# Kernel optimization log

Hardware: AMD Instinct MI355X
Metric: run time of the kernel (lower is better)

## Reference

```python
import math
import jax, jax.numpy as jnp
import numpy as np

D, H, L, DFF, V = 512, 8, 6, 2048, 32000
B, S = 2, 2048
PAD = 1


def _layernorm(x, g, b, eps=1e-5):
    m = x.mean(-1, keepdims=True)
    v = ((x - m) ** 2).mean(-1, keepdims=True)
    return (x - m) / jnp.sqrt(v + eps) * g + b


def _mha(qx, kx, w, b, mask, h=H):
    # w: [4, D, D] (q,k,v,out), b: [4, D]; mask broadcastable to [B,1,Sq,Sk]
    bs, sq, d = qx.shape
    dk = d // h
    def proj(x, i):
        return (x @ w[i] + b[i]).reshape(bs, -1, h, dk).transpose(0, 2, 1, 3)
    q, k, v = proj(qx, 0), proj(kx, 1), proj(kx, 2)
    scores = jnp.einsum('bhqd,bhkd->bhqk', q, k) / math.sqrt(dk)
    scores = jnp.where(mask, scores, -jnp.inf)
    attn = jax.nn.softmax(scores, axis=-1)
    out = jnp.einsum('bhqk,bhkd->bhqd', attn, v).transpose(0, 2, 1, 3).reshape(bs, sq, d)
    return out @ w[3] + b[3]


def _ff(x, w1, b1, w2, b2):
    return jax.nn.relu(x @ w1 + b1) @ w2 + b2


def _sinusoidal_pe(max_len, d):
    pos = np.arange(max_len)[:, None].astype(np.float64)
    div = np.exp(np.arange(0, d, 2) * (-math.log(10000.0) / d))
    pe = np.zeros((max_len, d), np.float32)
    pe[:, 0::2] = np.sin(pos * div)
    pe[:, 1::2] = np.cos(pos * div)
    return jnp.asarray(pe[None])  # [1, max_len, d]


def setup_inputs() -> dict:
    key = jax.random.key(0)
    ks = iter(jax.random.split(key, 32))
    def w(shape):
        return jax.random.normal(next(ks), shape, jnp.float32) * 0.02
    inp = {
        'src': jax.random.randint(next(ks), (B, S), 2, V),
        'tgt': jax.random.randint(next(ks), (B, S), 2, V),
        'src_emb': w((V, D)),
        'tgt_emb': w((V, D)),
        'pe': _sinusoidal_pe(S, D),
        'enc_attn_w': w((L, 4, D, D)), 'enc_attn_b': jnp.zeros((L, 4, D)),
        'enc_ff_w1': w((L, D, DFF)), 'enc_ff_b1': jnp.zeros((L, DFF)),
        'enc_ff_w2': w((L, DFF, D)), 'enc_ff_b2': jnp.zeros((L, D)),
        'enc_ln_g': jnp.ones((L, 2, D)), 'enc_ln_b': jnp.zeros((L, 2, D)),
        'dec_self_w': w((L, 4, D, D)), 'dec_self_b': jnp.zeros((L, 4, D)),
        'dec_src_w': w((L, 4, D, D)), 'dec_src_b': jnp.zeros((L, 4, D)),
        'dec_ff_w1': w((L, D, DFF)), 'dec_ff_b1': jnp.zeros((L, DFF)),
        'dec_ff_w2': w((L, DFF, D)), 'dec_ff_b2': jnp.zeros((L, D)),
        'dec_ln_g': jnp.ones((L, 3, D)), 'dec_ln_b': jnp.zeros((L, 3, D)),
        'ln_g': jnp.ones((D,)), 'ln_b': jnp.zeros((D,)),
        'fc_w': w((D, V)), 'fc_b': jnp.zeros((V,)),
    }
    return inp


def reference(src, tgt, src_emb, tgt_emb, pe,
              enc_attn_w, enc_attn_b, enc_ff_w1, enc_ff_b1, enc_ff_w2, enc_ff_b2,
              enc_ln_g, enc_ln_b,
              dec_self_w, dec_self_b, dec_src_w, dec_src_b,
              dec_ff_w1, dec_ff_b1, dec_ff_w2, dec_ff_b2, dec_ln_g, dec_ln_b,
              ln_g, ln_b, fc_w, fc_b):
    s_len, t_len = src.shape[1], tgt.shape[1]
    src_mask = (src != PAD)[:, None, None, :]                      # [B,1,1,Ss]
    tril = jnp.tril(jnp.ones((t_len, t_len), bool))
    tgt_mask = (tgt != PAD)[:, None, None, :] & tril[None, None]   # [B,1,St,St]

    x = src_emb[src] + pe[:, :s_len]
    for l in range(L):
        x2 = _layernorm(x, enc_ln_g[l, 0], enc_ln_b[l, 0])
        x = x + _mha(x2, x2, enc_attn_w[l], enc_attn_b[l], src_mask)
        x2 = _layernorm(x, enc_ln_g[l, 1], enc_ln_b[l, 1])
        x = x + _ff(x2, enc_ff_w1[l], enc_ff_b1[l], enc_ff_w2[l], enc_ff_b2[l])
    memory = x

    y = tgt_emb[tgt] + pe[:, :t_len]
    for l in range(L):
        y2 = _layernorm(y, dec_ln_g[l, 0], dec_ln_b[l, 0])
        y = y + _mha(y2, y2, dec_self_w[l], dec_self_b[l], tgt_mask)
        y2 = _layernorm(y, dec_ln_g[l, 1], dec_ln_b[l, 1])
        y = y + _mha(y2, memory, dec_src_w[l], dec_src_b[l], src_mask)
        y2 = _layernorm(y, dec_ln_g[l, 2], dec_ln_b[l, 2])
        y = y + _ff(y2, dec_ff_w1[l], dec_ff_b1[l], dec_ff_w2[l], dec_ff_b2[l])

    return _layernorm(y, ln_g, ln_b) @ fc_w + fc_b  # [B, St, V]
```

## Files before the change

### kernel.cpp

```cpp
#include <hip/hip_runtime.h>
#include <math.h>

#define D_MODEL 512
#define NHEAD   8
#define NLAYER  6
#define DFF_    2048
#define VOCAB   32000
#define BATCH   2
#define SEQ     2048
#define NTOK    (BATCH*SEQ)
#define PAD_ID  1

typedef __attribute__((ext_vector_type(8))) short s16x8;
typedef __attribute__((ext_vector_type(4))) float f32x4;
typedef unsigned short u16;
typedef unsigned int   u32;
typedef unsigned long long u64;

__device__ __forceinline__ u16 f2bf(float x) {
  u32 u = __builtin_bit_cast(u32, x);
  u += 0x7FFFu + ((u >> 16) & 1u);
  return (u16)(u >> 16);
}

__device__ __forceinline__ float exp2i(float x) {
  float r; asm("v_exp_f32 %0, %1" : "=v"(r) : "v"(x)); return r;
}

__device__ __forceinline__ void gload16(const void* g, void* l) {
  __builtin_amdgcn_global_load_lds(
      (const __attribute__((address_space(1))) u32*)g,
      (__attribute__((address_space(3))) u32*)l, 16, 0, 0);
}

#define CEXP 0.1803368802f

__global__ __launch_bounds__(256) void embed2_kernel(
    const int* __restrict__ src, const int* __restrict__ tgt,
    const float* __restrict__ se, const float* __restrict__ te,
    const float* __restrict__ pe, float* __restrict__ xe, float* __restrict__ yd)
{
  const int z = blockIdx.y;
  const int* tok = z ? tgt : src;
  const float* emb = z ? te : se;
  float* out = z ? yd : xe;
  const int total = NTOK * D_MODEL;
  for (int i = blockIdx.x * 256 + threadIdx.x; i < total; i += gridDim.x * 256) {
    int t = i >> 9;
    int d = i & 511;
    int s = t & (SEQ - 1);
    out[i] = emb[(size_t)tok[t] * D_MODEL + d] + pe[(size_t)s * D_MODEL + d];
  }
}

__global__ __launch_bounds__(64) void padmask2_kernel(
    const int* __restrict__ src, const int* __restrict__ tgt,
    u64* __restrict__ pmS, u64* __restrict__ pmT)
{
  const int z = blockIdx.z;
  const int* tok = z ? tgt : src;
  u64* pm = z ? pmT : pmS;
  int b = blockIdx.y, t = blockIdx.x;
  int lane = threadIdx.x;
  u64 m = __ballot(tok[(size_t)b * SEQ + t * 64 + lane] != PAD_ID);
  if (lane == 0) pm[b * (SEQ / 64) + t] = m;
}

__global__ __launch_bounds__(256) void ln_kernel(
    const float* __restrict__ x, const float* __restrict__ g,
    const float* __restrict__ bb, u16* __restrict__ y)
{
  __shared__ float red[8];
  const size_t row = blockIdx.x;
  const float* xr = x + row * D_MODEL;
  u16* yr = y + row * D_MODEL;
  const int t = threadIdx.x;
  float a0 = xr[t], a1 = xr[t + 256];
  float s = a0 + a1;
  #pragma unroll
  for (int o = 32; o > 0; o >>= 1) s += __shfl_down(s, o, 64);
  int wv = t >> 6, ln = t & 63;
  if (ln == 0) red[wv] = s;
  __syncthreads();
  if (t == 0) red[4] = red[0] + red[1] + red[2] + red[3];
  __syncthreads();
  float mean = red[4] * (1.0f / D_MODEL);
  float d0 = a0 - mean, d1 = a1 - mean;
  float vs = d0 * d0 + d1 * d1;
  #pragma unroll
  for (int o = 32; o > 0; o >>= 1) vs += __shfl_down(vs, o, 64);
  if (ln == 0) red[wv] = vs;
  __syncthreads();
  if (t == 0) red[5] = red[0] + red[1] + red[2] + red[3];
  __syncthreads();
  float inv = rsqrtf(red[5] * (1.0f / D_MODEL) + 1e-5f);
  yr[t]       = f2bf(d0 * inv * g[t]       + bb[t]);
  yr[t + 256] = f2bf(d1 * inv * g[t + 256] + bb[t + 256]);
}

__global__ __launch_bounds__(256) void tconv2_kernel(
    const float* __restrict__ s0, const float* __restrict__ s1,
    u16* __restrict__ d0, u16* __restrict__ d1, int zsplit, int K, int N)
{
  __shared__ float tile[64][65];
  const int z = blockIdx.z;
  const float* src = (z < zsplit) ? s0 + (size_t)z * K * N : s1 + (size_t)(z - zsplit) * K * N;
  u16* dst = (z < zsplit) ? d0 + (size_t)z * K * N : d1 + (size_t)(z - zsplit) * K * N;
  const int n0 = blockIdx.x * 64, k0 = blockIdx.y * 64;
  const int t = threadIdx.x;
  const int cr = t >> 4, cc = (t & 15) * 4;
  #pragma unroll
  for (int it = 0; it < 4; ++it) {
    int kr = cr + it * 16;
    float4 v = *(const float4*)&src[(size_t)(k0 + kr) * N + n0 + cc];
    tile[kr][cc] = v.x; tile[kr][cc + 1] = v.y; tile[kr][cc + 2] = v.z; tile[kr][cc + 3] = v.w;
  }
  __syncthreads();
  #pragma unroll
  for (int it = 0; it < 4; ++it) {
    int nr = cr + it * 16;
    u32 lo = (u32)f2bf(tile[cc + 0][nr]) | ((u32)f2bf(tile[cc + 1][nr]) << 16);
    u32 hi = (u32)f2bf(tile[cc + 2][nr]) | ((u32)f2bf(tile[cc + 3][nr]) << 16);
    uint2 pk; pk.x = lo; pk.y = hi;
    *(uint2*)&dst[(size_t)(n0 + nr) * K + k0 + cc] = pk;
  }
}

template<int MODE, int BM, int BN, int MAP>
__global__ __launch_bounds__(256, 2) void mm_kernel(
    const u16* __restrict__ A, const u16* __restrict__ Wt,
    const float* __restrict__ bias, const float* __restrict__ res,
    void* __restrict__ Cout, u16* __restrict__ vtOut,
    int M, int N, int K,
    long long wStride, long long bStride, long long cStride)
{
  constexpr int MI = BM / 32;
  constexpr int NI = BN / 32;
  constexpr bool DB = (BM == 64 && BN == 64);
  __shared__ u16 sh[(DB ? 2 : 1) * (BM + BN) * 64];
  const int z = blockIdx.z;
  size_t wOff, bOff;
  if (MAP == 1) {
    wOff = (size_t)(z >> 1) * 4 * 262144 + (size_t)(1 + (z & 1)) * 262144;
    bOff = (size_t)(z >> 1) * 4 * 512 + (size_t)(1 + (z & 1)) * 512;
  } else {
    wOff = (size_t)z * wStride;
    bOff = (size_t)z * bStride;
  }
  Wt += wOff;
  bias += bOff;
  const int bm = blockIdx.y * BM, bn = blockIdx.x * BN;
  const int tid = threadIdx.x, lane = tid & 63, w = tid >> 6;
  const int wm = w >> 1, wn = w & 1;
  const int l15 = lane & 15, l4 = lane >> 4;
  const int wrow0 = wm * (BM / 2), wcol0 = wn * (BN / 2);
  const u16* aBase = A  + (size_t)bm * K;
  const u16* bBase = Wt + (size_t)bn * K;
  f32x4 acc[MI][NI] = {};

  auto mfma_step = [&](const u16* Asb, const u16* Bsb) {
    #pragma unroll
    for (int ks = 0; ks < 2; ++ks) {
      s16x8 af[MI], bf[NI];
      #pragma unroll
      for (int mi = 0; mi < MI; ++mi) {
        int rr = wrow0 + mi * 16 + l15;
        af[mi] = *(const s16x8*)&Asb[(rr << 6) + (((ks * 4 + l4) ^ (rr & 7)) << 3)];
      }
      #pragma unroll
      for (int ni = 0; ni < NI; ++ni) {
        int rr = wcol0 + ni * 16 + l15;
        bf[ni] = *(const s16x8*)&Bsb[(rr << 6) + (((ks * 4 + l4) ^ (rr & 7)) << 3)];
      }
      #pragma unroll
      for (int mi = 0; mi < MI; ++mi)
        #pragma unroll
        for (int ni = 0; ni < NI; ++ni)
          acc[mi][ni] = __builtin_amdgcn_mfma_f32_16x16x32_bf16(af[mi], bf[ni], acc[mi][ni], 0, 0, 0);
    }
  };

  if constexpr (DB) {
    u16* As0 = sh;
    u16* As1 = sh + 64 * 64;
    u16* Bs0 = sh + 2 * 64 * 64;
    u16* Bs1 = sh + 3 * 64 * 64;
    auto stage = [&](int k0, u16* Ad, u16* Bd) {
      #pragma unroll
      for (int i = 0; i < 2; ++i) {
        int lin = i * 256 + tid;
        int r = lin >> 3, sp = lin & 7;
        gload16(aBase + (size_t)r * K + k0 + ((sp ^ (r & 7)) * 8), &Ad[(i * 256 + w * 64) * 8]);
      }
      #pragma unroll
      for (int i = 0; i < 2; ++i) {
        int lin = i * 256 + tid;
        int r = lin >> 3, sp = lin & 7;
        gload16(bBase + (size_t)r * K + k0 + ((sp ^ (r & 7)) * 8), &Bd[(i * 256 + w * 64) * 8]);
      }
    };
    stage(0, As0, Bs0);
    __syncthreads();
    const int nt = K >> 6;
    for (int t = 0; t < nt; ++t) {
      const bool even = !(t & 1);
      u16* Ac = even ? As0 : As1;
      u16* Bc = even ? Bs0 : Bs1;
      if (t + 1 < nt) stage((t + 1) << 6, even ? As1 : As0, even ? Bs1 : Bs0);
      mfma_step(Ac, Bc);
      __syncthreads();
    }
  } else {
    u16* As = sh;
    u16* Bs = sh + BM * 64;
    for (int k0 = 0; k0 < K; k0 += 64) {
      #pragma unroll
      for (int i = 0; i < BM / 32; ++i) {
        int lin = i * 256 + tid;
        int r = lin >> 3, sp = lin & 7;
        gload16(aBase + (size_t)r * K + k0 + ((sp ^ (r & 7)) * 8), &As[(i * 256 + w * 64) * 8]);
      }
      #pragma unroll
      for (int i = 0; i < BN / 32; ++i) {
        int lin = i * 256 + tid;
        int r = lin >> 3, sp = lin & 7;
        gload16(bBase + (size_t)r * K + k0 + ((sp ^ (r & 7)) * 8), &Bs[(i * 256 + w * 64) * 8]);
      }
      __syncthreads();
      mfma_step(As, Bs);
      __syncthreads();
    }
  }

  const bool vpath = (MODE == 4 && z == 2) || (MODE == 5 && (z & 1) == 1);
  if (vpath) {
    u16* TT = sh;
    #pragma unroll
    for (int mi = 0; mi < MI; ++mi)
      #pragma unroll
      for (int ni = 0; ni < NI; ++ni)
        #pragma unroll
        for (int r = 0; r < 4; ++r) {
          int rowl = wrow0 + mi * 16 + l4 * 4 + r;
          int coll = wcol0 + ni * 16 + l15;
          TT[coll * 72 + rowl] = f2bf(acc[mi][ni][r] + bias[bn + coll]);
        }
    __syncthreads();
    const int b = bm >> 11, s0loc = bm & 2047, h = bn >> 6;
    const int layer = (MODE == 5) ? (z >> 1) : 0;
    u16* vbase = vtOut + (size_t)layer * ((size_t)NTOK * D_MODEL)
               + ((size_t)(b * NHEAD + h) * 64) * SEQ;
    int d = tid >> 2, sc = (tid & 3) * 16;
    s16x8 v0 = *(const s16x8*)&TT[d * 72 + sc];
    s16x8 v1 = *(const s16x8*)&TT[d * 72 + sc + 8];
    *(s16x8*)(vbase + (size_t)d * SEQ + s0loc + sc) = v0;
    *(s16x8*)(vbase + (size_t)d * SEQ + s0loc + sc + 8) = v1;
    return;
  }

  const int zi = (MAP == 1) ? (z >> 1) : z;
  #pragma unroll
  for (int ni = 0; ni < NI; ++ni) {
    int col = bn + wcol0 + ni * 16 + l15;
    float bb = bias[col];
    #pragma unroll
    for (int mi = 0; mi < MI; ++mi) {
      #pragma unroll
      for (int r = 0; r < 4; ++r) {
        int row = bm + wrow0 + mi * 16 + l4 * 4 + r;
        size_t off = (size_t)zi * cStride + (size_t)row * N + col;
        float v = acc[mi][ni][r] + bb;
        if (MODE == 1 || MODE == 6) v += res[(size_t)row * N + col];
        if (MODE == 3) v = fmaxf(v, 0.0f);
        if (MODE <= 1 || MODE == 6) ((float*)Cout)[off] = v;
        else                        ((u16*)Cout)[off] = f2bf(v);
        if (MODE == 6) vtOut[(size_t)row * N + col] = f2bf(v);
      }
    }
  }
}

template<int CAUSAL>
__global__ __launch_bounds__(256, 2) void fattn_kernel(
    const u16* __restrict__ Qg, const u16* __restrict__ Kg,
    const u16* __restrict__ Vt, const u64* __restrict__ padm,
    u16* __restrict__ Og)
{
  __shared__ u16 Ks[2][128 * 64];
  __shared__ u16 Vs[2][64 * 128];
  __shared__ u16 Ps[4][16 * 128];
  const int qtile = CAUSAL ? (int)(gridDim.x - 1 - blockIdx.x) : (int)blockIdx.x;
  const int qt = qtile * 64;
  const int h = blockIdx.y, b = blockIdx.z;
  const int tid = threadIdx.x, lane = tid & 63, w = tid >> 6;
  const int l15 = lane & 15, l4 = lane >> 4;
  const int hoff = h * 64;
  const u16* Kbase = Kg + (size_t)(b * SEQ) * D_MODEL + hoff;
  const u16* Vbase = Vt + (size_t)(b * NHEAD + h) * 64 * SEQ;
  const u64* pmb = padm + b * (SEQ / 64);

  s16x8 aq[2];
  {
    const u16* qp = Qg + (size_t)(b * SEQ + qt + w * 16 + l15) * D_MODEL + hoff + l4 * 8;
    aq[0] = *(const s16x8*)qp;
    aq[1] = *(const s16x8*)(qp + 32);
  }

  f32x4 oacc[4] = {};
  float mrow[4] = {-1e30f, -1e30f, -1e30f, -1e30f};
  float lrow[4] = {0.f, 0.f, 0.f, 0.f};
  const int nt = CAUSAL ? (qt >> 7) + 1 : SEQ / 128;

  #define STAGE(KV0, BUF)                                                              \
    {                                                                                  \
      _Pragma("unroll")                                                                \
      for (int it = 0; it < 4; ++it) {                                                 \
        int lin = it * 256 + tid;                                                      \
        int rr = lin >> 3, sp = lin & 7;                                               \
        gload16(Kbase + (size_t)((KV0) + rr) * D_MODEL + ((sp ^ (rr & 7)) * 8),        \
                &Ks[BUF][(it * 256 + w * 64) * 8]);                                    \
      }                                                                                \
      _Pragma("unroll")                                                                \
      for (int it = 0; it < 4; ++it) {                                                 \
        int lin = it * 256 + tid;                                                      \
        int rr = lin >> 4, ko = lin & 15;                                              \
        gload16(Vbase + (size_t)rr * SEQ + (KV0) + ((ko ^ (rr & 15)) * 8),             \
                &Vs[BUF][(it * 256 + w * 64) * 8]);                                    \
      }                                                                                \
    }

  STAGE(0, 0);
  __syncthreads();

  for (int kt = 0; kt < nt; ++kt) {
    const int kv0 = kt * 128;
    const int cur = kt & 1;
    if (kt + 1 < nt) STAGE(kv0 + 128, cur ^ 1);

    f32x4 sac[8] = {};
    #pragma unroll
    for (int ks = 0; ks < 2; ++ks)
      #pragma unroll
      for (int jn = 0; jn < 8; ++jn) {
        int rr = jn * 16 + l15;
        s16x8 bk = *(const s16x8*)&Ks[cur][(rr << 6) + (((ks * 4 + l4) ^ (rr & 7)) << 3)];
        sac[jn] = __builtin_amdgcn_mfma_f32_16x16x32_bf16(aq[ks], bk, sac[jn], 0, 0, 0);
      }

    const u64 m0 = pmb[(kv0 >> 6)];
    const u64 m1 = pmb[(kv0 >> 6) + 1];
    const bool lastC = CAUSAL && (kt == nt - 1);
    if (((m0 & m1) != ~0ull) || lastC) {
      #pragma unroll
      for (int jn = 0; jn < 8; ++jn) {
        int kvg = kv0 + jn * 16 + l15;
        u64 mm = (jn < 4) ? m0 : m1;
        bool okp = (mm >> ((jn & 3) * 16 + l15)) & 1;
        #pragma unroll
        for (int r = 0; r < 4; ++r) {
          int qg = qt + w * 16 + l4 * 4 + r;
          bool ok = okp && (!CAUSAL || kvg <= qg);
          if (!ok) sac[jn][r] = -1e30f;
        }
      }
    }

    float mx[4];
    #pragma unroll
    for (int r = 0; r < 4; ++r) {
      float m = fmaxf(fmaxf(fmaxf(sac[0][r], sac[1][r]), fmaxf(sac[2][r], sac[3][r])),
                      fmaxf(fmaxf(sac[4][r], sac[5][r]), fmaxf(sac[6][r], sac[7][r])));
      #pragma unroll
      for (int o = 1; o < 16; o <<= 1) m = fmaxf(m, __shfl_xor(m, o, 16));
      mx[r] = m;
    }
    float growth = fmaxf(fmaxf(mx[0] - mrow[0], mx[1] - mrow[1]),
                         fmaxf(mx[2] - mrow[2], mx[3] - mrow[3]));
    if (__any(growth > 64.0f)) {
      #pragma unroll
      for (int r = 0; r < 4; ++r) {
        float mn = fmaxf(mrow[r], mx[r]);
        float sc = exp2i((mrow[r] - mn) * CEXP);
        mrow[r] = mn;
        lrow[r] *= sc;
        #pragma unroll
        for (int jn = 0; jn < 4; ++jn) oacc[jn][r] *= sc;
      }
    }

    #pragma unroll
    for (int r = 0; r < 4; ++r) {
      const int prow = l4 * 4 + r;
      float rs = 0.f;
      #pragma unroll
      for (int jn = 0; jn < 8; ++jn) {
        float pv = exp2i((sac[jn][r] - mrow[r]) * CEXP);
        rs += pv;
        int g = ((jn * 2 + (l15 >> 3)) ^ prow) & 15;
        Ps[w][prow * 128 + g * 8 + (l15 & 7)] = f2bf(pv);
      }
      #pragma unroll
      for (int o = 1; o < 16; o <<= 1) rs += __shfl_xor(rs, o, 16);
      lrow[r] += rs;
    }

    #pragma unroll
    for (int kslot = 0; kslot < 4; ++kslot) {
      s16x8 pa = *(const s16x8*)&Ps[w][l15 * 128 + ((((kslot * 4 + l4) ^ l15) & 15) << 3)];
      #pragma unroll
      for (int jn = 0; jn < 4; ++jn) {
        int rr = jn * 16 + l15;
        s16x8 bv = *(const s16x8*)&Vs[cur][(rr << 7) + (((kslot * 4 + l4) ^ (rr & 15)) << 3)];
        oacc[jn] = __builtin_amdgcn_mfma_f32_16x16x32_bf16(pa, bv, oacc[jn], 0, 0, 0);
      }
    }
    __syncthreads();
  }
  #undef STAGE

  float inv[4];
  #pragma unroll
  for (int r = 0; r < 4; ++r) inv[r] = 1.0f / lrow[r];
  #pragma unroll
  for (int jn = 0; jn < 4; ++jn)
    #pragma unroll
    for (int r = 0; r < 4; ++r)
      Og[(size_t)(b * SEQ + qt + w * 16 + l4 * 4 + r) * D_MODEL + hoff + jn * 16 + l15] =
          f2bf(oacc[jn][r] * inv[r]);
}

extern "C" void kernel_launch(void* const* d_in, const int* in_sizes, int n_in,
                              void* d_out, int out_size, void* d_ws, size_t ws_size,
                              hipStream_t stream)
{
  const int*   src        = (const int*)  d_in[0];
  const int*   tgt        = (const int*)  d_in[1];
  const float* src_emb    = (const float*)d_in[2];
  const float* tgt_emb    = (const float*)d_in[3];
  const float* pe         = (const float*)d_in[4];
  const float* enc_attn_w = (const float*)d_in[5];
  const float* enc_attn_b = (const float*)d_in[6];
  const float* enc_ff_w1  = (const float*)d_in[7];
  const float* enc_ff_b1  = (const float*)d_in[8];
  const float* enc_ff_w2  = (const float*)d_in[9];
  const float* enc_ff_b2  = (const float*)d_in[10];
  const float* enc_ln_g   = (const float*)d_in[11];
  const float* enc_ln_bb  = (const float*)d_in[12];
  const float* dec_self_w = (const float*)d_in[13];
  const float* dec_self_b = (const float*)d_in[14];
  const float* dec_src_w  = (const float*)d_in[15];
  const float* dec_src_b  = (const float*)d_in[16];
  const float* dec_ff_w1  = (const float*)d_in[17];
  const float* dec_ff_b1  = (const float*)d_in[18];
  const float* dec_ff_w2  = (const float*)d_in[19];
  const float* dec_ff_b2  = (const float*)d_in[20];
  const float* dec_ln_g   = (const float*)d_in[21];
  const float* dec_ln_bb  = (const float*)d_in[22];
  const float* fin_ln_g   = (const float*)d_in[23];
  const float* fin_ln_b   = (const float*)d_in[24];
  const float* fc_w       = (const float*)d_in[25];
  const float* fc_b       = (const float*)d_in[26];
  float* out = (float*)d_out;

  const size_t DD = (size_t)D_MODEL * D_MODEL;
  const size_t FD = (size_t)D_MODEL * DFF_;
  const size_t TD = (size_t)NTOK * D_MODEL;

  char* ob = (char*)d_out;
  size_t off = 0;
  auto alloco = [&](size_t bytes) { void* p = ob + off; off += (bytes + 255) & ~(size_t)255; return p; };
  u16* wt_enc_attn = (u16*)alloco(24 * DD * 2);
  u16* wt_dec_self = (u16*)alloco(24 * DD * 2);
  u16* wt_dec_src  = (u16*)alloco(24 * DD * 2);
  u16* wt_enc_ff1  = (u16*)alloco(6 * FD * 2);
  u16* wt_enc_ff2  = (u16*)alloco(6 * FD * 2);
  u16* wt_dec_ff1  = (u16*)alloco(6 * FD * 2);
  u16* wt_dec_ff2  = (u16*)alloco(6 * FD * 2);
  u16* qb   = (u16*)alloco(2 * TD * 2);
  u16* kb   = qb + TD;
  u16* vtb  = (u16*)alloco(TD * 2);
  u16* aob  = (u16*)alloco(TD * 2);
  u16* hbb  = (u16*)alloco((size_t)NTOK * DFF_ * 2);
  u16* memb = (u16*)alloco(TD * 2);
  u16* ckb  = (u16*)alloco(6 * TD * 2);
  u16* cvtb = (u16*)alloco(6 * TD * 2);

  char* wsb = (char*)d_ws;
  u16*   fcwt = (u16*)wsb;
  size_t wo = ((size_t)VOCAB * D_MODEL * 2 + 255) & ~(size_t)255;
  float* xe  = (float*)(wsb + wo); wo += TD * 4;
  float* yd  = (float*)(wsb + wo); wo += TD * 4;
  u16*   x2b = (u16*)(wsb + wo);   wo += TD * 2;
  u64*   pmS = (u64*)(wsb + wo);   wo += 1024;
  u64*   pmT = (u64*)(wsb + wo);

  dim3 blk(256);
  dim3 gN512(8, 64, 1), gQKV(8, 64, 3), gCKV(8, 64, 12);
  dim3 gFF1(16, 32, 1), gFC(250, 32, 1);
  dim3 gAttn(SEQ / 64, NHEAD, BATCH);
  const long long llDD = (long long)DD, llTD = (long long)TD;

  padmask2_kernel<<<dim3(SEQ / 64, BATCH, 2), dim3(64), 0, stream>>>(src, tgt, pmS, pmT);
  tconv2_kernel<<<dim3(8, 8, 48), blk, 0, stream>>>(enc_attn_w, dec_self_w, wt_enc_attn, wt_dec_self, 24, 512, 512);
  tconv2_kernel<<<dim3(8, 8, 24), blk, 0, stream>>>(dec_src_w, dec_src_w, wt_dec_src, wt_dec_src, 24, 512, 512);
  tconv2_kernel<<<dim3(32, 8, 12), blk, 0, stream>>>(enc_ff_w1, dec_ff_w1, wt_enc_ff1, wt_dec_ff1, 6, 512, 2048);
  tconv2_kernel<<<dim3(8, 32, 12), blk, 0, stream>>>(enc_ff_w2, dec_ff_w2, wt_enc_ff2, wt_dec_ff2, 6, 2048, 512);
  tconv2_kernel<<<dim3(500, 8, 1), blk, 0, stream>>>(fc_w, fc_w, fcwt, fcwt, 1, 512, VOCAB);
  embed2_kernel<<<dim3(2048, 2), blk, 0, stream>>>(src, tgt, src_emb, tgt_emb, pe, xe, yd);

  for (int l = 0; l < NLAYER; ++l) {
    ln_kernel<<<dim3(NTOK), blk, 0, stream>>>(xe, enc_ln_g + (size_t)(l * 2 + 0) * D_MODEL,
                                              enc_ln_bb + (size_t)(l * 2 + 0) * D_MODEL, x2b);
    mm_kernel<4, 64, 64, 0><<<gQKV, blk, 0, stream>>>(x2b, wt_enc_attn + (size_t)l * 4 * DD,
        enc_attn_b + (size_t)l * 4 * D_MODEL, nullptr, qb, vtb, NTOK, 512, 512, llDD, D_MODEL, llTD);
    fattn_kernel<0><<<gAttn, blk, 0, stream>>>(qb, kb, vtb, pmS, aob);
    mm_kernel<1, 64, 64, 0><<<gN512, blk, 0, stream>>>(aob, wt_enc_attn + (size_t)(l * 4 + 3) * DD,
        enc_attn_b + (size_t)(l * 4 + 3) * D_MODEL, xe, xe, nullptr, NTOK, 512, 512, 0, 0, 0);
    ln_kernel<<<dim3(NTOK), blk, 0, stream>>>(xe, enc_ln_g + (size_t)(l * 2 + 1) * D_MODEL,
                                              enc_ln_bb + (size_t)(l * 2 + 1) * D_MODEL, x2b);
    mm_kernel<3, 128, 128, 0><<<gFF1, blk, 0, stream>>>(x2b, wt_enc_ff1 + (size_t)l * FD,
        enc_ff_b1 + (size_t)l * DFF_, nullptr, hbb, nullptr, NTOK, DFF_, 512, 0, 0, 0);
    if (l == NLAYER - 1)
      mm_kernel<6, 64, 64, 0><<<gN512, blk, 0, stream>>>(hbb, wt_enc_ff2 + (size_t)l * FD,
          enc_ff_b2 + (size_t)l * D_MODEL, xe, xe, memb, NTOK, 512, DFF_, 0, 0, 0);
    else
      mm_kernel<1, 64, 64, 0><<<gN512, blk, 0, stream>>>(hbb, wt_enc_ff2 + (size_t)l * FD,
          enc_ff_b2 + (size_t)l * D_MODEL, xe, xe, nullptr, NTOK, 512, DFF_, 0, 0, 0);
  }

  mm_kernel<5, 64, 64, 1><<<gCKV, blk, 0, stream>>>(memb, wt_dec_src, dec_src_b, nullptr,
      ckb, cvtb, NTOK, 512, 512, 0, 0, llTD);

  for (int l = 0; l < NLAYER; ++l) {
    const u16* Ws = wt_dec_self + (size_t)l * 4 * DD;
    const u16* Wc = wt_dec_src + (size_t)l * 4 * DD;
    const float* bs  = dec_self_b + (size_t)l * 4 * D_MODEL;
    const float* bcb = dec_src_b + (size_t)l * 4 * D_MODEL;
    ln_kernel<<<dim3(NTOK), blk, 0, stream>>>(yd, dec_ln_g + (size_t)(l * 3 + 0) * D_MODEL,
                                              dec_ln_bb + (size_t)(l * 3 + 0) * D_MODEL, x2b);
    mm_kernel<4, 64, 64, 0><<<gQKV, blk, 0, stream>>>(x2b, Ws, bs, nullptr, qb, vtb,
                                                      NTOK, 512, 512, llDD, D_MODEL, llTD);
    fattn_kernel<1><<<gAttn, blk, 0, stream>>>(qb, kb, vtb, pmT, aob);
    mm_kernel<1, 64, 64, 0><<<gN512, blk, 0, stream>>>(aob, Ws + 3 * DD, bs + 3 * D_MODEL, yd, yd,
                                                       nullptr, NTOK, 512, 512, 0, 0, 0);
    ln_kernel<<<dim3(NTOK), blk, 0, stream>>>(yd, dec_ln_g + (size_t)(l * 3 + 1) * D_MODEL,
                                              dec_ln_bb + (size_t)(l * 3 + 1) * D_MODEL, x2b);
    mm_kernel<2, 64, 64, 0><<<gN512, blk, 0, stream>>>(x2b, Wc, bcb, nullptr, qb, nullptr,
                                                       NTOK, 512, 512, 0, 0, 0);
    fattn_kernel<0><<<gAttn, blk, 0, stream>>>(qb, ckb + (size_t)l * TD, cvtb + (size_t)l * TD,
                                               pmS, aob);
    mm_kernel<1, 64, 64, 0><<<gN512, blk, 0, stream>>>(aob, Wc + 3 * DD, bcb + 3 * D_MODEL, yd, yd,
                                                       nullptr, NTOK, 512, 512, 0, 0, 0);
    ln_kernel<<<dim3(NTOK), blk, 0, stream>>>(yd, dec_ln_g + (size_t)(l * 3 + 2) * D_MODEL,
                                              dec_ln_bb + (size_t)(l * 3 + 2) * D_MODEL, x2b);
    mm_kernel<3, 128, 128, 0><<<gFF1, blk, 0, stream>>>(x2b, wt_dec_ff1 + (size_t)l * FD,
        dec_ff_b1 + (size_t)l * DFF_, nullptr, hbb, nullptr, NTOK, DFF_, 512, 0, 0, 0);
    mm_kernel<1, 64, 64, 0><<<gN512, blk, 0, stream>>>(hbb, wt_dec_ff2 + (size_t)l * FD,
        dec_ff_b2 + (size_t)l * D_MODEL, yd, yd, nullptr, NTOK, 512, DFF_, 0, 0, 0);
  }

  ln_kernel<<<dim3(NTOK), blk, 0, stream>>>(yd, fin_ln_g, fin_ln_b, x2b);
  mm_kernel<0, 128, 128, 0><<<gFC, blk, 0, stream>>>(x2b, fcwt, fc_b, nullptr, out, nullptr,
                                                     NTOK, VOCAB, 512, 0, 0, 0);

  (void)in_sizes; (void)n_in; (void)out_size; (void)ws_size;
}
```

Measured before the change: 2.504 ms.

## Fuse cross-attn Q projection into attention, merge weight transposes, widen FC tile

The decoder cross-attention Q projection is now computed inside the flash-attention kernel from the normalized activations and the per-head weight slice, which removes a separate GEMM launch and the Q round trip through global memory. The three attention-weight transpose launches are merged into one kernel, which assumes the three weight buffers are contiguous in the destination. The final vocab projection uses 128x256 tiles with half the grid. Risks include extra per-block work and shared-memory syncs in the attention prologue, and higher register pressure from the wider FC tile.

```diff
diff --git a/kernel.cpp b/kernel.cpp
--- a/kernel.cpp
+++ b/kernel.cpp
@@ -123,6 +123,36 @@
     u32 hi = (u32)f2bf(tile[cc + 2][nr]) | ((u32)f2bf(tile[cc + 3][nr]) << 16);
     uint2 pk; pk.x = lo; pk.y = hi;
     *(uint2*)&dst[(size_t)(n0 + nr) * K + k0 + cc] = pk;
+  }
+}
+
+__global__ __launch_bounds__(256) void tconv3_kernel(
+    const float* __restrict__ s0, const float* __restrict__ s1,
+    const float* __restrict__ s2, u16* __restrict__ dst0)
+{
+  __shared__ float tile[64][65];
+  const int z = blockIdx.z;
+  const float* src = (z < 24) ? s0 + (size_t)z * 262144
+                   : (z < 48) ? s1 + (size_t)(z - 24) * 262144
+                              : s2 + (size_t)(z - 48) * 262144;
+  u16* dst = dst0 + (size_t)z * 262144;
+  const int n0 = blockIdx.x * 64, k0 = blockIdx.y * 64;
+  const int t = threadIdx.x;
+  const int cr = t >> 4, cc = (t & 15) * 4;
+  #pragma unroll
+  for (int it = 0; it < 4; ++it) {
+    int kr = cr + it * 16;
+    float4 v = *(const float4*)&src[(size_t)(k0 + kr) * 512 + n0 + cc];
+    tile[kr][cc] = v.x; tile[kr][cc + 1] = v.y; tile[kr][cc + 2] = v.z; tile[kr][cc + 3] = v.w;
+  }
+  __syncthreads();
+  #pragma unroll
+  for (int it = 0; it < 4; ++it) {
+    int nr = cr + it * 16;
+    u32 lo = (u32)f2bf(tile[cc + 0][nr]) | ((u32)f2bf(tile[cc + 1][nr]) << 16);
+    u32 hi = (u32)f2bf(tile[cc + 2][nr]) | ((u32)f2bf(tile[cc + 3][nr]) << 16);
+    uint2 pk; pk.x = lo; pk.y = hi;
+    *(uint2*)&dst[(size_t)(n0 + nr) * 512 + k0 + cc] = pk;
   }
 }
 
@@ -280,10 +310,11 @@
   }
 }
 
-template<int CAUSAL>
+template<int CAUSAL, int QPROJ>
 __global__ __launch_bounds__(256, 2) void fattn_kernel(
     const u16* __restrict__ Qg, const u16* __restrict__ Kg,
-    const u16* __restrict__ Vt, const u64* __restrict__ padm,
+    const u16* __restrict__ Vt, const u16* __restrict__ Wq,
+    const float* __restrict__ qbias, const u64* __restrict__ padm,
     u16* __restrict__ Og)
 {
   __shared__ u16 Ks[2][128 * 64];
@@ -300,7 +331,57 @@
   const u64* pmb = padm + b * (SEQ / 64);
 
   s16x8 aq[2];
-  {
+  if constexpr (QPROJ) {
+    const u16* xBase = Qg + (size_t)(b * SEQ + qt) * D_MODEL;
+    const u16* wBase = Wq + (size_t)hoff * D_MODEL;
+    u16* Xs = Ks[0];
+    u16* Wsh = Ks[0] + 64 * 64;
+    f32x4 qa[4] = {};
+    for (int k0 = 0; k0 < 512; k0 += 64) {
+      #pragma unroll
+      for (int i = 0; i < 2; ++i) {
+        int lin = i * 256 + tid;
+        int r = lin >> 3, sp = lin & 7;
+        gload16(xBase + (size_t)r * D_MODEL + k0 + ((sp ^ (r & 7)) * 8), &Xs[(i * 256 + w * 64) * 8]);
+      }
+      #pragma unroll
+      for (int i = 0; i < 2; ++i) {
+        int lin = i * 256 + tid;
+        int r = lin >> 3, sp = lin & 7;
+        gload16(wBase + (size_t)r * D_MODEL + k0 + ((sp ^ (r & 7)) * 8), &Wsh[(i * 256 + w * 64) * 8]);
+      }
+      __syncthreads();
+      #pragma unroll
+      for (int ks = 0; ks < 2; ++ks) {
+        int rr = w * 16 + l15;
+        s16x8 xa = *(const s16x8*)&Xs[(rr << 6) + (((ks * 4 + l4) ^ (rr & 7)) << 3)];
+        #pragma unroll
+        for (int ni = 0; ni < 4; ++ni) {
+          int rw = ni * 16 + l15;
+          s16x8 wb = *(const s16x8*)&Wsh[(rw << 6) + (((ks * 4 + l4) ^ (rw & 7)) << 3)];
+          qa[ni] = __builtin_amdgcn_mfma_f32_16x16x32_bf16(xa, wb, qa[ni], 0, 0, 0);
+        }
+      }
+      __syncthreads();
+    }
+    u16* Qsh = (u16*)Ps;
+    #pragma unroll
+    for (int ni = 0; ni < 4; ++ni) {
+      int col = ni * 16 + l15;
+      float bb = qbias[hoff + col];
+      #pragma unroll
+      for (int r = 0; r < 4; ++r) {
+        int row = w * 16 + l4 * 4 + r;
+        Qsh[(row << 6) + ((((col >> 3)) ^ (row & 7)) << 3) + (col & 7)] = f2bf(qa[ni][r] + bb);
+      }
+    }
+    __syncthreads();
+    {
+      int rr = w * 16 + l15;
+      aq[0] = *(const s16x8*)&Qsh[(rr << 6) + (((0 + l4) ^ (rr & 7)) << 3)];
+      aq[1] = *(const s16x8*)&Qsh[(rr << 6) + (((4 + l4) ^ (rr & 7)) << 3)];
+    }
+  } else {
     const u16* qp = Qg + (size_t)(b * SEQ + qt + w * 16 + l15) * D_MODEL + hoff + l4 * 8;
     aq[0] = *(const s16x8*)qp;
     aq[1] = *(const s16x8*)(qp + 32);
@@ -329,6 +410,7 @@
       }                                                                                \
     }
 
+  if constexpr (QPROJ) __syncthreads();
   STAGE(0, 0);
   __syncthreads();
 
@@ -496,13 +578,12 @@
 
   dim3 blk(256);
   dim3 gN512(8, 64, 1), gQKV(8, 64, 3), gCKV(8, 64, 12);
-  dim3 gFF1(16, 32, 1), gFC(250, 32, 1);
+  dim3 gFF1(16, 32, 1), gFC(125, 32, 1);
   dim3 gAttn(SEQ / 64, NHEAD, BATCH);
   const long long llDD = (long long)DD, llTD = (long long)TD;
 
   padmask2_kernel<<<dim3(SEQ / 64, BATCH, 2), dim3(64), 0, stream>>>(src, tgt, pmS, pmT);
-  tconv2_kernel<<<dim3(8, 8, 48), blk, 0, stream>>>(enc_attn_w, dec_self_w, wt_enc_attn, wt_dec_self, 24, 512, 512);
-  tconv2_kernel<<<dim3(8, 8, 24), blk, 0, stream>>>(dec_src_w, dec_src_w, wt_dec_src, wt_dec_src, 24, 512, 512);
+  tconv3_kernel<<<dim3(8, 8, 72), blk, 0, stream>>>(enc_attn_w, dec_self_w, dec_src_w, wt_enc_attn);
   tconv2_kernel<<<dim3(32, 8, 12), blk, 0, stream>>>(enc_ff_w1, dec_ff_w1, wt_enc_ff1, wt_dec_ff1, 6, 512, 2048);
   tconv2_kernel<<<dim3(8, 32, 12), blk, 0, stream>>>(enc_ff_w2, dec_ff_w2, wt_enc_ff2, wt_dec_ff2, 6, 2048, 512);
   tconv2_kernel<<<dim3(500, 8, 1), blk, 0, stream>>>(fc_w, fc_w, fcwt, fcwt, 1, 512, VOCAB);
@@ -513,7 +594,7 @@
                                               enc_ln_bb + (size_t)(l * 2 + 0) * D_MODEL, x2b);
     mm_kernel<4, 64, 64, 0><<<gQKV, blk, 0, stream>>>(x2b, wt_enc_attn + (size_t)l * 4 * DD,
         enc_attn_b + (size_t)l * 4 * D_MODEL, nullptr, qb, vtb, NTOK, 512, 512, llDD, D_MODEL, llTD);
-    fattn_kernel<0><<<gAttn, blk, 0, stream>>>(qb, kb, vtb, pmS, aob);
+    fattn_kernel<0, 0><<<gAttn, blk, 0, stream>>>(qb, kb, vtb, nullptr, nullptr, pmS, aob);
     mm_kernel<1, 64, 64, 0><<<gN512, blk, 0, stream>>>(aob, wt_enc_attn + (size_t)(l * 4 + 3) * DD,
         enc_attn_b + (size_t)(l * 4 + 3) * D_MODEL, xe, xe, nullptr, NTOK, 512, 512, 0, 0, 0);
     ln_kernel<<<dim3(NTOK), blk, 0, stream>>>(xe, enc_ln_g + (size_t)(l * 2 + 1) * D_MODEL,
@@ -540,15 +621,13 @@
                                               dec_ln_bb + (size_t)(l * 3 + 0) * D_MODEL, x2b);
     mm_kernel<4, 64, 64, 0><<<gQKV, blk, 0, stream>>>(x2b, Ws, bs, nullptr, qb, vtb,
                                                       NTOK, 512, 512, llDD, D_MODEL, llTD);
-    fattn_kernel<1><<<gAttn, blk, 0, stream>>>(qb, kb, vtb, pmT, aob);
+    fattn_kernel<1, 0><<<gAttn, blk, 0, stream>>>(qb, kb, vtb, nullptr, nullptr, pmT, aob);
     mm_kernel<1, 64, 64, 0><<<gN512, blk, 0, stream>>>(aob, Ws + 3 * DD, bs + 3 * D_MODEL, yd, yd,
                                                        nullptr, NTOK, 512, 512, 0, 0, 0);
     ln_kernel<<<dim3(NTOK), blk, 0, stream>>>(yd, dec_ln_g + (size_t)(l * 3 + 1) * D_MODEL,
                                               dec_ln_bb + (size_t)(l * 3 + 1) * D_MODEL, x2b);
-    mm_kernel<2, 64, 64, 0><<<gN512, blk, 0, stream>>>(x2b, Wc, bcb, nullptr, qb, nullptr,
-                                                       NTOK, 512, 512, 0, 0, 0);
-    fattn_kernel<0><<<gAttn, blk, 0, stream>>>(qb, ckb + (size_t)l * TD, cvtb + (size_t)l * TD,
-                                               pmS, aob);
+    fattn_kernel<0, 1><<<gAttn, blk, 0, stream>>>(x2b, ckb + (size_t)l * TD, cvtb + (size_t)l * TD,
+                                                  Wc, bcb, pmS, aob);
     mm_kernel<1, 64, 64, 0><<<gN512, blk, 0, stream>>>(aob, Wc + 3 * DD, bcb + 3 * D_MODEL, yd, yd,
                                                        nullptr, NTOK, 512, 512, 0, 0, 0);
     ln_kernel<<<dim3(NTOK), blk, 0, stream>>>(yd, dec_ln_g + (size_t)(l * 3 + 2) * D_MODEL,
@@ -560,7 +639,7 @@
   }
 
   ln_kernel<<<dim3(NTOK), blk, 0, stream>>>(yd, fin_ln_g, fin_ln_b, x2b);
-  mm_kernel<0, 128, 128, 0><<<gFC, blk, 0, stream>>>(x2b, fcwt, fc_b, nullptr, out, nullptr,
+  mm_kernel<0, 128, 256, 0><<<gFC, blk, 0, stream>>>(x2b, fcwt, fc_b, nullptr, out, nullptr,
                                                      NTOK, VOCAB, 512, 0, 0, 0);
 
   (void)in_sizes; (void)n_in; (void)out_size; (void)ws_size;
```

Result: no change. 2.503 ms (-0.0%).
